# Kernel optimization log

Measured on AMD Instinct MI355X. Metric: run time of the kernel, lower is better.

The kernel has to match this reference:

```python
import jax, jax.numpy as jnp
import numpy as np

B, C, O, H, W = 4, 64, 64, 128, 128
KH = KW = 3
K = KH * KW  # 9 kernel positions
MRM = 10.0   # max_residue_magnitude


def setup_inputs() -> dict:
    key = jax.random.key(0)
    ks = jax.random.split(key, 6)
    return {
        "x_main": jax.random.normal(ks[0], (B, C, H, W), jnp.float32),
        "x_extra": jax.random.normal(ks[1], (B, C, H, W), jnp.float32),
        "pre_offset": jax.random.normal(ks[2], (B, K, H, W, 2), jnp.float32) * 2.0,
        "pre_sim": jax.random.uniform(ks[3], (B, K, H, W), jnp.float32),
        "weight": jax.random.normal(ks[4], (O, C, KH, KW), jnp.float32) / np.sqrt(C * K),
        "bias": jnp.zeros((O,), jnp.float32),
        "w_om": jax.random.normal(ks[5], (3 * K, C, KH, KW), jnp.float32) * 0.01,
        "b_om": jnp.zeros((3 * K,), jnp.float32),
    }


def _bilinear(img, py, px):
    """img: [C,Hi,Wi]; py, px: [K,Ho,Wo] float sample coords. Zero padding outside."""
    Hi, Wi = img.shape[1], img.shape[2]
    y0 = jnp.floor(py)
    x0 = jnp.floor(px)
    dy = py - y0  # [K,Ho,Wo]
    dx = px - x0

    def gather(yi, xi):
        valid = ((yi >= 0) & (yi <= Hi - 1) & (xi >= 0) & (xi <= Wi - 1)).astype(img.dtype)
        yc = jnp.clip(yi, 0, Hi - 1).astype(jnp.int32)
        xc = jnp.clip(xi, 0, Wi - 1).astype(jnp.int32)
        return img[:, yc, xc] * valid[None]  # [C,K,Ho,Wo]

    v00 = gather(y0, x0)
    v01 = gather(y0, x0 + 1)
    v10 = gather(y0 + 1, x0)
    v11 = gather(y0 + 1, x0 + 1)
    return (v00 * (1 - dy) * (1 - dx) + v01 * (1 - dy) * dx
            + v10 * dy * (1 - dx) + v11 * dy * dx)


def reference(x_main, x_extra, pre_offset, pre_sim, weight, bias, w_om, b_om):
    # conv_offset_mask: 3x3, stride 1, pad 1 -> [B, 3K, H, W]
    out = jax.lax.conv_general_dilated(
        x_extra, w_om, (1, 1), ((1, 1), (1, 1)),
        dimension_numbers=("NCHW", "OIHW", "NCHW")) + b_om[None, :, None, None]
    o1, o2, mask = jnp.split(out, 3, axis=1)  # each [B,K,H,W]
    offset = MRM * jnp.tanh(jnp.concatenate([o1, o2], axis=1))  # [B,2K,H,W]
    # pre_offset reorder: even channels <- pre_offset[...,1] (y), odd <- pre_offset[...,0] (x)
    off_y = offset[:, 0::2] + pre_offset[..., 1]  # [B,K,H,W]
    off_x = offset[:, 1::2] + pre_offset[..., 0]
    mask = jax.nn.sigmoid(mask * pre_sim)  # use_sim=True

    f32 = offset.dtype
    ky = (jnp.arange(K) // KW).astype(f32)  # kernel row per position k
    kx = (jnp.arange(K) % KW).astype(f32)   # kernel col per position k
    # base grid: p = out_pos*stride - pad + k*dil = h - 1 + ky (stride=1,pad=1,dil=1)
    py = off_y + (jnp.arange(H, dtype=f32)[None, None, :, None] - 1.0) + ky[None, :, None, None]
    px = off_x + (jnp.arange(W, dtype=f32)[None, None, None, :] - 1.0) + kx[None, :, None, None]

    sampled = jax.vmap(_bilinear)(x_main, py, px)      # [B,C,K,H,W]
    sampled = sampled * mask[:, None]                   # modulated (DCNv2)
    y = jnp.einsum("bckhw,ock->bohw", sampled, weight.reshape(O, C, K))
    return y + bias[None, :, None, None]
```

## Files before the change

### kernel.cpp

```cpp
#include <hip/hip_runtime.h>
#include <math.h>

#define Bn 4
#define Cn 64
#define On 64
#define Hn 128
#define Wn 128
#define Kn 9
#define HWn (Hn*Wn)
#define ZROW 16384
#define XBSTRIDE (16385*64)

typedef _Float16 v8h __attribute__((ext_vector_type(8)));
typedef _Float16 v2h __attribute__((ext_vector_type(2)));
typedef float v4f __attribute__((ext_vector_type(4)));

__device__ inline unsigned short f2h(float f) {
  _Float16 h = (_Float16)f;
  return __builtin_bit_cast(unsigned short, h);
}
__device__ inline _Float16 u2h(unsigned v) {
  return __builtin_bit_cast(_Float16, (unsigned short)(v & 0xffff));
}
__device__ inline v8h sp8(_Float16 x) { v8h v = {x,x,x,x,x,x,x,x}; return v; }

__global__ __launch_bounds__(256) void k_prep(
    const float* __restrict__ x_main,
    const float* __restrict__ x_extra,
    const float* __restrict__ weight,
    const float* __restrict__ w_om,
    _Float16* __restrict__ xT,
    _Float16* __restrict__ xeF,
    _Float16* __restrict__ Wfrag,
    _Float16* __restrict__ WOMfrag)
{
  const int blk = blockIdx.x;
  const int t = threadIdx.x;

  if (blk < 2048) {
    __shared__ float tile[64 * 65];
    int isExtra = blk >> 10;
    int b  = (blk >> 8) & 3;
    int p0 = (blk & 255) << 6;
    const float* src = (isExtra ? x_extra : x_main) + b * Cn * HWn + p0;
    #pragma unroll
    for (int i = 0; i < 4; ++i) {
      int c  = i * 16 + (t >> 4);
      int p4 = (t & 15) * 4;
      float4 v = *(const float4*)(src + c * HWn + p4);
      tile[c * 65 + p4 + 0] = v.x;
      tile[c * 65 + p4 + 1] = v.y;
      tile[c * 65 + p4 + 2] = v.z;
      tile[c * 65 + p4 + 3] = v.w;
    }
    __syncthreads();
    _Float16* dst = (isExtra ? xeF : xT) + b * XBSTRIDE + p0 * 64;
    #pragma unroll
    for (int i = 0; i < 8; ++i) {
      int p  = i * 8 + (t >> 5);
      int c2 = (t & 31) * 2;
      v2h pk = { (_Float16)tile[c2 * 65 + p], (_Float16)tile[(c2 + 1) * 65 + p] };
      *(v2h*)(dst + p * 64 + c2) = pk;
    }
  } else {
    int rb = blk - 2048;
    for (int idx = rb * 256 + t; idx < 36864; idx += 64 * 256) {
      int j  = idx & 7;
      int ln = (idx >> 3) & 63;
      int hk = (idx >> 9) & 1;
      int ot = (idx >> 10) & 3;
      int k  = idx >> 12;
      int o = ot * 16 + (ln & 15);
      int c = hk * 32 + (ln >> 4) * 8 + j;
      Wfrag[idx] = (_Float16)weight[(o * Cn + c) * Kn + k];
    }
    for (int idx = rb * 256 + t; idx < 18432; idx += 64 * 256) {
      int j    = idx & 7;
      int ln   = (idx >> 3) & 63;
      int jt   = (idx >> 9) & 1;
      int half = (idx >> 10) & 1;
      int k9   = idx >> 11;
      int jo = jt * 16 + (ln & 15);
      int c  = half * 32 + (ln >> 4) * 8 + j;
      float v = (jo < 27) ? w_om[(jo * Cn + c) * Kn + k9] : 0.f;
      WOMfrag[idx] = (_Float16)v;
    }
    if (rb == 0 && t < 256) {
      int b = t >> 6, c = t & 63;
      xT[b * XBSTRIDE + ZROW * 64 + c] = (_Float16)0.f;
      xeF[b * XBSTRIDE + ZROW * 64 + c] = (_Float16)0.f;
    }
  }
}

__global__ __launch_bounds__(256, 4) void k_fused(
    const _Float16* __restrict__ xT,
    const _Float16* __restrict__ xeF,
    const _Float16* __restrict__ Wfrag,
    const _Float16* __restrict__ WOMfrag,
    const float* __restrict__ pre_offset,
    const float* __restrict__ pre_sim,
    const float* __restrict__ b_om,
    const float* __restrict__ bias,
    float* __restrict__ out)
{
  __shared__ float jbuf[4 * 16 * 36];
  __shared__ uint4 recbuf[4 * 16 * 9];

  const int t    = threadIdx.x;
  const int lane = t & 63;
  const int wv   = __builtin_amdgcn_readfirstlane(t >> 6);
  const int raw  = blockIdx.x;
  const int blk  = ((raw & 7) << 7) | (raw >> 3);
  const int b    = blk >> 8;
  const int h    = (blk >> 1) & 127;
  const int wq   = (blk & 1) * 4 + wv;
  const int kq   = lane >> 4;
  const int n    = lane & 15;
  const int w    = wq * 16 + n;

  unsigned tapoff[9];
  #pragma unroll
  for (int k9 = 0; k9 < 9; ++k9) {
    int r  = h - 1 + k9 / 3;
    int cc = w - 1 + k9 % 3;
    bool v = ((unsigned)r < (unsigned)Hn) & ((unsigned)cc < (unsigned)Wn);
    tapoff[k9] = (v ? (unsigned)(r * Wn + cc) : (unsigned)ZROW) * 64u;
  }

  const _Float16* xe = xeF + b * XBSTRIDE;
  const v8h* Wom = (const v8h*)WOMfrag;
  v4f ca0 = {0,0,0,0}, ca1 = {0,0,0,0};
  for (int k9 = 0; k9 < 9; ++k9) {
    #pragma unroll
    for (int half = 0; half < 2; ++half) {
      int abase = ((k9 * 2 + half) * 2) * 64 + lane;
      v8h A0 = Wom[abase];
      v8h A1 = Wom[abase + 64];
      v8h Bt = *(const v8h*)(xe + tapoff[k9] + half * 32 + kq * 8);
      ca0 = __builtin_amdgcn_mfma_f32_16x16x32_f16(A0, Bt, ca0, 0, 0, 0);
      ca1 = __builtin_amdgcn_mfma_f32_16x16x32_f16(A1, Bt, ca1, 0, 0, 0);
    }
  }

  float* jb = jbuf + wv * (16 * 36);
  *(v4f*)(jb + n * 36 + kq * 4)      = ca0;
  *(v4f*)(jb + n * 36 + 16 + kq * 4) = ca1;

  uint4* rb = recbuf + wv * (16 * 9);
  if (kq < 3) {
    #pragma unroll
    for (int kk = 0; kk < 3; ++kk) {
      int k = kq * 3 + kk;
      float sy = jb[n * 36 + 2 * k]     + b_om[2 * k];
      float sx = jb[n * 36 + 2 * k + 1] + b_om[2 * k + 1];
      float sm = jb[n * 36 + 18 + k]    + b_om[18 + k];
      int pbase = ((b * Kn + k) * Hn + h) * Wn + w;
      float2 po = *(const float2*)(pre_offset + pbase * 2);
      float ey = __expf(2.f * sy);
      float ex = __expf(2.f * sx);
      float py = 10.f - 20.f / (ey + 1.f) + po.y + (float)(h - 1 + k / 3);
      float px = 10.f - 20.f / (ex + 1.f) + po.x + (float)(w - 1 + k % 3);
      float m  = 1.f / (1.f + __expf(-sm * pre_sim[pbase]));
      float fy = floorf(py), fx = floorf(px);
      float dy = py - fy, dx = px - fx;
      int y0 = (int)fy, x0 = (int)fx;
      int y1 = y0 + 1, x1 = x0 + 1;
      bool vy0 = (y0 >= 0) & (y0 < Hn), vy1 = (y1 >= 0) & (y1 < Hn);
      bool vx0 = (x0 >= 0) & (x0 < Wn), vx1 = (x1 >= 0) & (x1 < Wn);
      unsigned r00 = (vy0 & vx0) ? (unsigned)(y0 * Wn + x0) : ZROW;
      unsigned r01 = (vy0 & vx1) ? (unsigned)(y0 * Wn + x1) : ZROW;
      unsigned r10 = (vy1 & vx0) ? (unsigned)(y1 * Wn + x0) : ZROW;
      unsigned r11 = (vy1 & vx1) ? (unsigned)(y1 * Wn + x1) : ZROW;
      float wy0 = 1.f - dy, wx0 = 1.f - dx;
      uint4 rec;
      rec.x = r00 | (r01 << 16);
      rec.y = r10 | (r11 << 16);
      rec.z = (unsigned)f2h(wy0 * wx0 * m) | ((unsigned)f2h(wy0 * dx * m) << 16);
      rec.w = (unsigned)f2h(dy * wx0 * m) | ((unsigned)f2h(dy * dx * m) << 16);
      rb[n * 9 + k] = rec;
    }
  }

  v4f acc0 = {0,0,0,0}, acc1 = {0,0,0,0}, acc2 = {0,0,0,0}, acc3 = {0,0,0,0};
  const _Float16* xb = xT + b * XBSTRIDE;
  const v8h* Wf = (const v8h*)Wfrag;

  uint4 rec0   = rb[n * 9 + 0];
  uint4 rec_nx = rb[n * 9 + 1];
  _Float16 h00 = u2h(rec0.z), h01 = u2h(rec0.z >> 16);
  _Float16 h10 = u2h(rec0.w), h11 = u2h(rec0.w >> 16);
  unsigned o00 = (rec0.x & 0xffff) * 64u + kq * 8;
  unsigned o01 = (rec0.x >> 16)    * 64u + kq * 8;
  unsigned o10 = (rec0.y & 0xffff) * 64u + kq * 8;
  unsigned o11 = (rec0.y >> 16)    * 64u + kq * 8;
  v8h C0 = *(const v8h*)(xb + o00);
  v8h C1 = *(const v8h*)(xb + o01);
  v8h C2 = *(const v8h*)(xb + o10);
  v8h C3 = *(const v8h*)(xb + o11);

  #pragma unroll
  for (int k = 0; k < 9; ++k) {
    v8h H0 = *(const v8h*)(xb + o00 + 32);
    v8h H1 = *(const v8h*)(xb + o01 + 32);
    v8h H2 = *(const v8h*)(xb + o10 + 32);
    v8h H3 = *(const v8h*)(xb + o11 + 32);

    v8h N0, N1, N2, N3;
    _Float16 nh00 = (_Float16)0.f, nh01 = (_Float16)0.f;
    _Float16 nh10 = (_Float16)0.f, nh11 = (_Float16)0.f;
    unsigned p00 = 0, p01 = 0, p10 = 0, p11 = 0;
    if (k < 8) {
      nh00 = u2h(rec_nx.z); nh01 = u2h(rec_nx.z >> 16);
      nh10 = u2h(rec_nx.w); nh11 = u2h(rec_nx.w >> 16);
      p00 = (rec_nx.x & 0xffff) * 64u + kq * 8;
      p01 = (rec_nx.x >> 16)    * 64u + kq * 8;
      p10 = (rec_nx.y & 0xffff) * 64u + kq * 8;
      p11 = (rec_nx.y >> 16)    * 64u + kq * 8;
      N0 = *(const v8h*)(xb + p00);
      N1 = *(const v8h*)(xb + p01);
      N2 = *(const v8h*)(xb + p10);
      N3 = *(const v8h*)(xb + p11);
    }
    uint4 rec_nx2 = rec_nx;
    if (k < 7) rec_nx2 = rb[n * 9 + k + 2];

    __builtin_amdgcn_sched_barrier(0);

    const v8h* wk = Wf + (k * 8) * 64 + lane;
    v8h A0 = wk[0 * 64], A1 = wk[1 * 64], A2 = wk[2 * 64], A3 = wk[3 * 64];
    v8h A4 = wk[4 * 64], A5 = wk[5 * 64], A6 = wk[6 * 64], A7 = wk[7 * 64];

    v8h Bf0 = C0 * sp8(h00) + C1 * sp8(h01) + C2 * sp8(h10) + C3 * sp8(h11);
    v8h Bf1 = H0 * sp8(h00) + H1 * sp8(h01) + H2 * sp8(h10) + H3 * sp8(h11);

    acc0 = __builtin_amdgcn_mfma_f32_16x16x32_f16(A0, Bf0, acc0, 0, 0, 0);
    acc1 = __builtin_amdgcn_mfma_f32_16x16x32_f16(A2, Bf0, acc1, 0, 0, 0);
    acc2 = __builtin_amdgcn_mfma_f32_16x16x32_f16(A4, Bf0, acc2, 0, 0, 0);
    acc3 = __builtin_amdgcn_mfma_f32_16x16x32_f16(A6, Bf0, acc3, 0, 0, 0);
    acc0 = __builtin_amdgcn_mfma_f32_16x16x32_f16(A1, Bf1, acc0, 0, 0, 0);
    acc1 = __builtin_amdgcn_mfma_f32_16x16x32_f16(A3, Bf1, acc1, 0, 0, 0);
    acc2 = __builtin_amdgcn_mfma_f32_16x16x32_f16(A5, Bf1, acc2, 0, 0, 0);
    acc3 = __builtin_amdgcn_mfma_f32_16x16x32_f16(A7, Bf1, acc3, 0, 0, 0);

    if (k < 8) {
      C0 = N0; C1 = N1; C2 = N2; C3 = N3;
      h00 = nh00; h01 = nh01; h10 = nh10; h11 = nh11;
      o00 = p00; o01 = p01; o10 = p10; o11 = p11;
      rec_nx = rec_nx2;
    }
  }

  const float4* b4 = (const float4*)bias;
  float4 vb0 = b4[0 * 4 + kq], vb1 = b4[1 * 4 + kq];
  float4 vb2 = b4[2 * 4 + kq], vb3 = b4[3 * 4 + kq];
  float* ob = out + (b * On) * HWn + h * Wn + wq * 16 + n;
  #pragma unroll
  for (int reg = 0; reg < 4; ++reg) {
    ob[(0 * 16 + kq * 4 + reg) * HWn] = acc0[reg] + ((const float*)&vb0)[reg];
    ob[(1 * 16 + kq * 4 + reg) * HWn] = acc1[reg] + ((const float*)&vb1)[reg];
    ob[(2 * 16 + kq * 4 + reg) * HWn] = acc2[reg] + ((const float*)&vb2)[reg];
    ob[(3 * 16 + kq * 4 + reg) * HWn] = acc3[reg] + ((const float*)&vb3)[reg];
  }
}

extern "C" void kernel_launch(void* const* d_in, const int* in_sizes, int n_in,
                              void* d_out, int out_size, void* d_ws, size_t ws_size,
                              hipStream_t stream) {
  const float* x_main     = (const float*)d_in[0];
  const float* x_extra    = (const float*)d_in[1];
  const float* pre_offset = (const float*)d_in[2];
  const float* pre_sim    = (const float*)d_in[3];
  const float* weight     = (const float*)d_in[4];
  const float* bias       = (const float*)d_in[5];
  const float* w_om       = (const float*)d_in[6];
  const float* b_om       = (const float*)d_in[7];
  float* out = (float*)d_out;

  char* ws = (char*)d_ws;
  _Float16* xT      = (_Float16*)(ws);
  _Float16* xeF     = (_Float16*)(ws + 8389120);
  _Float16* Wfrag   = (_Float16*)(ws + 16778240);
  _Float16* WOMfrag = (_Float16*)(ws + 16851968);

  k_prep<<<2112, 256, 0, stream>>>(x_main, x_extra, weight, w_om,
                                   xT, xeF, Wfrag, WOMfrag);
  k_fused<<<1024, 256, 0, stream>>>(xT, xeF, Wfrag, WOMfrag,
                                    pre_offset, pre_sim, b_om, bias, out);
}
```

Measured before the change: 151.0 us.

## Stage main-conv weight fragments in double-buffered LDS shared across waves

The weight fragments for each kernel position are now loaded from global memory once per block, by one rotating wave, into a double-buffered shared-memory tile. Previously every wave read them from global/L2 separately. All waves then read A operands from LDS, and the fragment packing order is changed to match. The aim is to cut redundant global weight traffic and register pressure, at the cost of a block-wide barrier per kernel position, extra LDS use (16KB) that may lower occupancy, and a serialized load on a single wave.

After: 145.0 us. 1.04x faster.

```diff
diff --git a/kernel.cpp b/kernel.cpp
--- a/kernel.cpp
+++ b/kernel.cpp
@@ -67,8 +67,8 @@
     for (int idx = rb * 256 + t; idx < 36864; idx += 64 * 256) {
       int j  = idx & 7;
       int ln = (idx >> 3) & 63;
-      int hk = (idx >> 9) & 1;
-      int ot = (idx >> 10) & 3;
+      int ot = (idx >> 9) & 3;
+      int hk = (idx >> 11) & 1;
       int k  = idx >> 12;
       int o = ot * 16 + (ln & 15);
       int c = hk * 32 + (ln >> 4) * 8 + j;
@@ -106,6 +106,7 @@
 {
   __shared__ float jbuf[4 * 16 * 36];
   __shared__ uint4 recbuf[4 * 16 * 9];
+  __shared__ __align__(16) _Float16 Abuf[2][8 * 512];
 
   const int t    = threadIdx.x;
   const int lane = t & 63;
@@ -186,6 +187,15 @@
   const _Float16* xb = xT + b * XBSTRIDE;
   const v8h* Wf = (const v8h*)Wfrag;
 
+  if (wv == 0) {
+    #pragma unroll
+    for (int f = 0; f < 8; ++f) {
+      v8h g = Wf[(0 * 8 + f) * 64 + lane];
+      *(v8h*)(&Abuf[0][f * 512 + lane * 8]) = g;
+    }
+  }
+  __syncthreads();
+
   uint4 rec0   = rb[n * 9 + 0];
   uint4 rec_nx = rb[n * 9 + 1];
   _Float16 h00 = u2h(rec0.z), h01 = u2h(rec0.z >> 16);
@@ -201,6 +211,13 @@
 
   #pragma unroll
   for (int k = 0; k < 9; ++k) {
+    if (k < 8 && wv == ((k + 1) & 3)) {
+      #pragma unroll
+      for (int f = 0; f < 8; ++f) {
+        v8h g = Wf[((k + 1) * 8 + f) * 64 + lane];
+        *(v8h*)(&Abuf[(k + 1) & 1][f * 512 + lane * 8]) = g;
+      }
+    }
     v8h H0 = *(const v8h*)(xb + o00 + 32);
     v8h H1 = *(const v8h*)(xb + o01 + 32);
     v8h H2 = *(const v8h*)(xb + o10 + 32);
@@ -227,27 +244,36 @@
 
     __builtin_amdgcn_sched_barrier(0);
 
-    const v8h* wk = Wf + (k * 8) * 64 + lane;
-    v8h A0 = wk[0 * 64], A1 = wk[1 * 64], A2 = wk[2 * 64], A3 = wk[3 * 64];
-    v8h A4 = wk[4 * 64], A5 = wk[5 * 64], A6 = wk[6 * 64], A7 = wk[7 * 64];
+    const v8h* Ab = (const v8h*)Abuf[k & 1];
+    v8h F0 = Ab[0 * 64 + lane], F1 = Ab[1 * 64 + lane];
+    v8h F2 = Ab[2 * 64 + lane], F3 = Ab[3 * 64 + lane];
 
     v8h Bf0 = C0 * sp8(h00) + C1 * sp8(h01) + C2 * sp8(h10) + C3 * sp8(h11);
+
+    acc0 = __builtin_amdgcn_mfma_f32_16x16x32_f16(F0, Bf0, acc0, 0, 0, 0);
+    acc1 = __builtin_amdgcn_mfma_f32_16x16x32_f16(F1, Bf0, acc1, 0, 0, 0);
+    acc2 = __builtin_amdgcn_mfma_f32_16x16x32_f16(F2, Bf0, acc2, 0, 0, 0);
+    acc3 = __builtin_amdgcn_mfma_f32_16x16x32_f16(F3, Bf0, acc3, 0, 0, 0);
+
+    v8h F4 = Ab[4 * 64 + lane], F5 = Ab[5 * 64 + lane];
+    v8h F6 = Ab[6 * 64 + lane], F7 = Ab[7 * 64 + lane];
     v8h Bf1 = H0 * sp8(h00) + H1 * sp8(h01) + H2 * sp8(h10) + H3 * sp8(h11);
 
-    acc0 = __builtin_amdgcn_mfma_f32_16x16x32_f16(A0, Bf0, acc0, 0, 0, 0);
-    acc1 = __builtin_amdgcn_mfma_f32_16x16x32_f16(A2, Bf0, acc1, 0, 0, 0);
-    acc2 = __builtin_amdgcn_mfma_f32_16x16x32_f16(A4, Bf0, acc2, 0, 0, 0);
-    acc3 = __builtin_amdgcn_mfma_f32_16x16x32_f16(A6, Bf0, acc3, 0, 0, 0);
-    acc0 = __builtin_amdgcn_mfma_f32_16x16x32_f16(A1, Bf1, acc0, 0, 0, 0);
-    acc1 = __builtin_amdgcn_mfma_f32_16x16x32_f16(A3, Bf1, acc1, 0, 0, 0);
-    acc2 = __builtin_amdgcn_mfma_f32_16x16x32_f16(A5, Bf1, acc2, 0, 0, 0);
-    acc3 = __builtin_amdgcn_mfma_f32_16x16x32_f16(A7, Bf1, acc3, 0, 0, 0);
+    acc0 = __builtin_amdgcn_mfma_f32_16x16x32_f16(F4, Bf1, acc0, 0, 0, 0);
+    acc1 = __builtin_amdgcn_mfma_f32_16x16x32_f16(F5, Bf1, acc1, 0, 0, 0);
+    acc2 = __builtin_amdgcn_mfma_f32_16x16x32_f16(F6, Bf1, acc2, 0, 0, 0);
+    acc3 = __builtin_amdgcn_mfma_f32_16x16x32_f16(F7, Bf1, acc3, 0, 0, 0);
 
     if (k < 8) {
       C0 = N0; C1 = N1; C2 = N2; C3 = N3;
       h00 = nh00; h01 = nh01; h10 = nh10; h11 = nh11;
       o00 = p00; o01 = p01; o10 = p10; o11 = p11;
       rec_nx = rec_nx2;
+    }
+
+    if (k < 8) {
+      asm volatile("s_waitcnt lgkmcnt(0)" ::: "memory");
+      __builtin_amdgcn_s_barrier();
     }
   }
 
```
